# Kernel optimization log

Measured on AMD Instinct MI355X. Metric: run time of the kernel, lower is better.

The kernel has to match this reference:

```python
import jax, jax.numpy as jnp
import numpy as np

L = 3        # number of GatedGCN layers
N = 30000    # nodes
E = 480000   # edges (avg degree 16)
D = 128      # hidden dim (= in_dim = out_dim)
IN = 128     # input feature dim
G = 64       # graphs in batch
C = 10       # classes


def setup_inputs() -> dict:
    key = jax.random.key(0)
    ks = jax.random.split(key, 32)
    s = 0.05  # weight scale to keep activations / sigmoid gates in a sane range
    inp = {
        "h": jax.random.normal(ks[0], (N, IN), jnp.float32),
        "e": jax.random.normal(ks[1], (E, IN), jnp.float32),
        "snorm_n": jax.random.uniform(ks[2], (N, 1), jnp.float32),
        "snorm_e": jax.random.uniform(ks[3], (E, 1), jnp.float32),
        "src": jax.random.randint(ks[4], (E,), 0, N, jnp.int32),
        "dst": jax.random.randint(ks[5], (E,), 0, N, jnp.int32),
        "graph_id": jnp.sort(jax.random.randint(ks[6], (N,), 0, G, jnp.int32)),
        # input embeddings
        "Wh_emb": jax.random.normal(ks[7], (IN, D), jnp.float32) * s,
        "bh_emb": jnp.zeros((D,), jnp.float32),
        "We_emb": jax.random.normal(ks[8], (IN, D), jnp.float32) * s,
        "be_emb": jnp.zeros((D,), jnp.float32),
        # per-layer A,B,C,D,E linears (stacked over L)
        "WA": jax.random.normal(ks[9], (L, D, D), jnp.float32) * s,
        "bA": jnp.zeros((L, D), jnp.float32),
        "WB": jax.random.normal(ks[10], (L, D, D), jnp.float32) * s,
        "bB": jnp.zeros((L, D), jnp.float32),
        "WC": jax.random.normal(ks[11], (L, D, D), jnp.float32) * s,
        "bC": jnp.zeros((L, D), jnp.float32),
        "WD": jax.random.normal(ks[12], (L, D, D), jnp.float32) * s,
        "bD": jnp.zeros((L, D), jnp.float32),
        "WE": jax.random.normal(ks[13], (L, D, D), jnp.float32) * s,
        "bE": jnp.zeros((L, D), jnp.float32),
        # batch-norm affine params (node / edge)
        "gn_h": jnp.ones((L, D), jnp.float32),
        "bt_h": jnp.zeros((L, D), jnp.float32),
        "gn_e": jnp.ones((L, D), jnp.float32),
        "bt_e": jnp.zeros((L, D), jnp.float32),
        # readout linear
        "Wr": jax.random.normal(ks[14], (D, C), jnp.float32) * s,
        "br": jnp.zeros((C,), jnp.float32),
    }
    return inp


def _bn(x, gamma, beta):
    # training-mode BatchNorm1d: biased batch stats over the node/edge axis
    mu = jnp.mean(x, axis=0)
    var = jnp.var(x, axis=0)
    return (x - mu) * jax.lax.rsqrt(var + 1e-5) * gamma + beta


def reference(h, e, snorm_n, snorm_e, src, dst, graph_id,
              Wh_emb, bh_emb, We_emb, be_emb,
              WA, bA, WB, bB, WC, bC, WD, bD, WE, bE,
              gn_h, bt_h, gn_e, bt_e, Wr, br):
    n_nodes = h.shape[0]
    h = h @ Wh_emb + bh_emb
    e = e @ We_emb + be_emb
    for l in range(WA.shape[0]):
        h_in, e_in = h, e
        Ah = h @ WA[l] + bA[l]
        Bh = h @ WB[l] + bB[l]
        Dh = h @ WD[l] + bD[l]
        Eh = h @ WE[l] + bE[l]
        Ce = e @ WC[l] + bC[l]
        # message: e_ij = Ce + Dh_src + Eh_dst ; gate = sigmoid(e_ij)
        e_new = Ce + Dh[src] + Eh[dst]                       # [E, D]
        sig = jax.nn.sigmoid(e_new)
        # reduce at dst: gated weighted mean of Bh_src
        num = jax.ops.segment_sum(sig * Bh[src], dst, num_segments=n_nodes)
        den = jax.ops.segment_sum(sig, dst, num_segments=n_nodes)
        h_new = Ah + num / (den + 1e-6)
        # graph norm
        h_new = h_new * snorm_n
        e_new = e_new * snorm_e
        # batch norm + ReLU + residual (dropout p=0 -> identity)
        h_new = jax.nn.relu(_bn(h_new, gn_h[l], bt_h[l]))
        e_new = jax.nn.relu(_bn(e_new, gn_e[l], bt_e[l]))
        h = h_in + h_new
        e = e_in + e_new
    # mean_nodes readout per graph, then linear classifier
    sums = jax.ops.segment_sum(h, graph_id, num_segments=G)
    cnt = jax.ops.segment_sum(jnp.ones((n_nodes, 1), h.dtype), graph_id, num_segments=G)
    hg = sums / jnp.maximum(cnt, 1.0)
    return hg @ Wr + br
```

## Files before the change

### kernel.cpp

```cpp
#include <hip/hip_runtime.h>
#include <cstdint>
#include <cstddef>

#define N_NODES  30000
#define N_EDGES  480000
#define N_LAYERS 3
#define N_GRAPHS 64
#define N_CLASS  10
#define NREP     32

typedef __attribute__((ext_vector_type(8))) short short8v;
typedef __attribute__((ext_vector_type(4))) float f32x4;

__device__ __forceinline__ unsigned short f2bf(float x) {
  union { float f; unsigned u; } v; v.f = x;
  unsigned r = v.u + 0x7FFFu + ((v.u >> 16) & 1u);
  return (unsigned short)(r >> 16);
}
__device__ __forceinline__ float bf2f(unsigned short h) {
  union { unsigned u; float f; } v; v.u = ((unsigned)h) << 16;
  return v.f;
}
__device__ __forceinline__ int swzW(int row, int off16) {
  return (row << 8) | (off16 ^ ((row & 7) << 4));
}

__global__ void wconv(const float* __restrict__ Wh, const float* __restrict__ We,
                      const float* __restrict__ WA, const float* __restrict__ WB,
                      const float* __restrict__ WC, const float* __restrict__ WD,
                      const float* __restrict__ WE, unsigned short* __restrict__ Wt)
{
  const int mi  = blockIdx.x >> 6;
  const int idx = (blockIdx.x & 63) * 256 + threadIdx.x;
  const float* src;
  if      (mi == 0) src = Wh;
  else if (mi == 1) src = We;
  else if (mi < 5)  src = WA + (size_t)(mi - 2) * 16384;
  else if (mi < 8)  src = WB + (size_t)(mi - 5) * 16384;
  else if (mi < 11) src = WC + (size_t)(mi - 8) * 16384;
  else if (mi < 14) src = WD + (size_t)(mi - 11) * 16384;
  else              src = WE + (size_t)(mi - 14) * 16384;
  const int k = idx >> 7, n = idx & 127;
  Wt[(size_t)mi * 16384 + (size_t)n * 128 + k] = f2bf(src[idx]);
}

struct GemmArgs {
  const unsigned short* Wt[4];
  const float* bias[4];
  unsigned short* out[4];
};

template<int NMAT, bool AFP32>
__global__ __launch_bounds__(256)
void gemm_mm(const void* __restrict__ Ap, GemmArgs g, int M)
{
  __shared__ __align__(16) unsigned char WL[32768];
  unsigned short* Wl = (unsigned short*)WL;
  const int t = threadIdx.x;
  const int w = t >> 6, l = t & 63;
  const int lr = l & 15, lkb = (l >> 4) * 8;
  const int r0 = blockIdx.x * 64;
  int arow = r0 + w * 16 + lr; if (arow >= M) arow = M - 1;

  short8v a[4];
  if (AFP32) {
    const float* A = (const float*)Ap;
#pragma unroll
    for (int kk = 0; kk < 4; ++kk) {
      const float* p = A + (size_t)arow * 128 + kk * 32 + lkb;
      const float4 u = *(const float4*)p;
      const float4 v = *(const float4*)(p + 4);
      short8v av;
      av[0]=f2bf(u.x); av[1]=f2bf(u.y); av[2]=f2bf(u.z); av[3]=f2bf(u.w);
      av[4]=f2bf(v.x); av[5]=f2bf(v.y); av[6]=f2bf(v.z); av[7]=f2bf(v.w);
      a[kk] = av;
    }
  } else {
    const unsigned short* A = (const unsigned short*)Ap;
#pragma unroll
    for (int kk = 0; kk < 4; ++kk)
      a[kk] = *(const short8v*)(A + (size_t)arow * 128 + kk * 32 + lkb);
  }

#pragma unroll
  for (int m = 0; m < NMAT; ++m) {
    if (m) __syncthreads();
#pragma unroll
    for (int p = 0; p < 8; ++p) {
      const int ci = t + p * 256;
      *(short8v*)(WL + swzW(ci >> 4, (ci & 15) * 16)) = *(const short8v*)(g.Wt[m] + (size_t)ci * 8);
    }
    __syncthreads();
    f32x4 acc[8];
#pragma unroll
    for (int ct = 0; ct < 8; ++ct) acc[ct] = (f32x4){0.f, 0.f, 0.f, 0.f};
#pragma unroll
    for (int kk = 0; kk < 4; ++kk)
#pragma unroll
      for (int ct = 0; ct < 8; ++ct) {
        const short8v b = *(const short8v*)(WL + swzW(ct * 16 + lr, kk * 64 + (l >> 4) * 16));
        acc[ct] = __builtin_amdgcn_mfma_f32_16x16x32_bf16(a[kk], b, acc[ct], 0, 0, 0);
      }
    __syncthreads();
#pragma unroll
    for (int ct = 0; ct < 8; ++ct) {
      const float bb = g.bias[m][ct * 16 + lr];
#pragma unroll
      for (int q = 0; q < 4; ++q)
        Wl[(w * 16 + (l >> 4) * 4 + q) * 136 + ct * 16 + lr] = f2bf(acc[ct][q] + bb);
    }
    __syncthreads();
    unsigned short* out = g.out[m];
#pragma unroll
    for (int p = 0; p < 4; ++p) {
      const int ci = t + p * 256;
      const int rr = ci >> 4, co = (ci & 15) * 8;
      const int grow = r0 + rr;
      if (grow < M)
        *(short8v*)(out + (size_t)grow * 128 + co) = *(const short8v*)(Wl + rr * 136 + co);
    }
  }
}

template<int LMODE>
__global__ __launch_bounds__(256)
void edge_fused(unsigned short* __restrict__ eres, unsigned short* __restrict__ enew,
                const unsigned short* __restrict__ WtC, const float* __restrict__ bC,
                const unsigned short* __restrict__ Dh, const unsigned short* __restrict__ Eh,
                const int* __restrict__ src, const int* __restrict__ dst,
                const float* __restrict__ snorm_e, const float2* __restrict__ pq)
{
  __shared__ __align__(16) unsigned char WL[32768];
  __shared__ float2 pql[128];
  unsigned short* Wl = (unsigned short*)WL;
  const int t = threadIdx.x;
  const int w = t >> 6, l = t & 63;
  const int lr = l & 15, lkb = (l >> 4) * 8;
  const int r0 = blockIdx.x * 64;
  if (LMODE >= 1 && t < 128) pql[t] = pq[t];
#pragma unroll
  for (int p = 0; p < 8; ++p) {
    const int ci = t + p * 256;
    *(short8v*)(WL + swzW(ci >> 4, (ci & 15) * 16)) = *(const short8v*)(WtC + (size_t)ci * 8);
  }
  __syncthreads();

  const int arow = r0 + w * 16 + lr;
  short8v a[4];
  if (LMODE == 0) {
#pragma unroll
    for (int kk = 0; kk < 4; ++kk)
      a[kk] = *(const short8v*)(eres + (size_t)arow * 128 + kk * 32 + lkb);
  } else {
    const float sn = snorm_e[arow];
#pragma unroll
    for (int kk = 0; kk < 4; ++kk) {
      const short8v ep = *(const short8v*)(enew + (size_t)arow * 128 + kk * 32 + lkb);
      const short8v er = *(const short8v*)(eres + (size_t)arow * 128 + kk * 32 + lkb);
      short8v av;
#pragma unroll
      for (int j = 0; j < 8; ++j) {
        const float2 PQ = pql[kk * 32 + lkb + j];
        const float x = bf2f((unsigned short)ep[j]) * sn * PQ.x + PQ.y;
        av[j] = (short)f2bf(bf2f((unsigned short)er[j]) + fmaxf(x, 0.f));
      }
      a[kk] = av;
      if (LMODE == 1)
        *(short8v*)(eres + (size_t)arow * 128 + kk * 32 + lkb) = av;
    }
  }

  f32x4 acc[8];
#pragma unroll
  for (int ct = 0; ct < 8; ++ct) acc[ct] = (f32x4){0.f, 0.f, 0.f, 0.f};
#pragma unroll
  for (int kk = 0; kk < 4; ++kk)
#pragma unroll
    for (int ct = 0; ct < 8; ++ct) {
      const short8v b = *(const short8v*)(WL + swzW(ct * 16 + lr, kk * 64 + (l >> 4) * 16));
      acc[ct] = __builtin_amdgcn_mfma_f32_16x16x32_bf16(a[kk], b, acc[ct], 0, 0, 0);
    }
  __syncthreads();
#pragma unroll
  for (int ct = 0; ct < 8; ++ct) {
    const float bb = bC[ct * 16 + lr];
#pragma unroll
    for (int q = 0; q < 4; ++q)
      Wl[(w * 16 + (l >> 4) * 4 + q) * 136 + ct * 16 + lr] = f2bf(acc[ct][q] + bb);
  }
  __syncthreads();
#pragma unroll
  for (int p = 0; p < 4; ++p) {
    const int ci = t + p * 256;
    const int rr = ci >> 4, co = (ci & 15) * 8;
    const int edge = r0 + rr;
    const int s = src[edge], d = dst[edge];
    const short8v ce = *(const short8v*)(Wl + rr * 136 + co);
    const short8v dv = *(const short8v*)(Dh + (size_t)s * 128 + co);
    const short8v ev = *(const short8v*)(Eh + (size_t)d * 128 + co);
    short8v ov;
#pragma unroll
    for (int j = 0; j < 8; ++j)
      ov[j] = (short)f2bf(bf2f((unsigned short)ce[j]) + bf2f((unsigned short)dv[j]) + bf2f((unsigned short)ev[j]));
    *(short8v*)(enew + (size_t)edge * 128 + co) = ov;
  }
}

__global__ void hist_kernel(const int* __restrict__ dst, int* __restrict__ cnt, int E)
{
  const int i = blockIdx.x * 256 + threadIdx.x;
  if (i < E) atomicAdd(&cnt[dst[i]], 1);
}

__global__ void scan_kernel(const int* __restrict__ cnt, int* __restrict__ start,
                            int* __restrict__ cursor, int n, int total)
{
  __shared__ int lds[1024];
  const int tid = threadIdx.x;
  const int chunk = (n + 1023) / 1024;
  const int lo = tid * chunk, hi = min(lo + chunk, n);
  int s = 0;
  for (int i = lo; i < hi; ++i) s += cnt[i];
  lds[tid] = s;
  __syncthreads();
  for (int off = 1; off < 1024; off <<= 1) {
    const int v = (tid >= off) ? lds[tid - off] : 0;
    __syncthreads();
    lds[tid] += v;
    __syncthreads();
  }
  int run = (tid == 0) ? 0 : lds[tid - 1];
  for (int i = lo; i < hi; ++i) { start[i] = run; cursor[i] = run; run += cnt[i]; }
  if (tid == 0) start[n] = total;
}

__global__ void scatter_kernel(const int* __restrict__ dst, int* __restrict__ cursor,
                               int* __restrict__ csr, int E)
{
  const int i = blockIdx.x * 256 + threadIdx.x;
  if (i < E) { const int p = atomicAdd(&cursor[dst[i]], 1); csr[p] = i; }
}

__global__ __launch_bounds__(256)
void aggregate(const unsigned short* __restrict__ enew, const unsigned short* __restrict__ Bh,
               const unsigned short* __restrict__ Ah, const float* __restrict__ snorm_n,
               const float* __restrict__ snorm_e, const int* __restrict__ start,
               const int* __restrict__ csr, const int* __restrict__ src,
               float* __restrict__ tbuf, float* __restrict__ statrep, int doE)
{
  __shared__ float2 red[16][132];
  const int t = threadIdx.x;
  const int g = t >> 4, q = t & 15;
  const int v = blockIdx.x * 16 + g;
  const int s0 = start[v], s1 = start[v + 1];
  float num[8] = {0,0,0,0,0,0,0,0}, den[8] = {0,0,0,0,0,0,0,0};
  float psE[8] = {0,0,0,0,0,0,0,0}, pqE[8] = {0,0,0,0,0,0,0,0};

  float sn = 0.f;
  short8v ev = {}, bv = {};
  if (s0 < s1) {
    const int eid = csr[s0];
    const int sv  = src[eid];
    sn = snorm_e[eid];
    ev = *(const short8v*)(enew + (size_t)eid * 128 + q * 8);
    bv = *(const short8v*)(Bh + (size_t)sv * 128 + q * 8);
  }
  for (int i = s0; i < s1; ++i) {
    float snn = 0.f;
    short8v evn = {}, bvn = {};
    if (i + 1 < s1) {
      const int eid = csr[i + 1];
      const int sv  = src[eid];
      snn = snorm_e[eid];
      evn = *(const short8v*)(enew + (size_t)eid * 128 + q * 8);
      bvn = *(const short8v*)(Bh + (size_t)sv * 128 + q * 8);
    }
#pragma unroll
    for (int j = 0; j < 8; ++j) {
      const float en = bf2f((unsigned short)ev[j]);
      const float sg = 1.f / (1.f + __expf(-en));
      num[j] = fmaf(sg, bf2f((unsigned short)bv[j]), num[j]);
      den[j] += sg;
      if (doE) { const float tv = en * sn; psE[j] += tv; pqE[j] = fmaf(tv, tv, pqE[j]); }
    }
    ev = evn; bv = bvn; sn = snn;
  }
  const float snv = snorm_n[v];
  const short8v av = *(const short8v*)(Ah + (size_t)v * 128 + q * 8);
  float hv[8];
#pragma unroll
  for (int j = 0; j < 8; ++j)
    hv[j] = (bf2f((unsigned short)av[j]) + num[j] / (den[j] + 1e-6f)) * snv;
  *(float4*)(tbuf + (size_t)v * 128 + q * 8)     = make_float4(hv[0], hv[1], hv[2], hv[3]);
  *(float4*)(tbuf + (size_t)v * 128 + q * 8 + 4) = make_float4(hv[4], hv[5], hv[6], hv[7]);

  float* rep = statrep + (size_t)(blockIdx.x & (NREP - 1)) * 512;
#pragma unroll
  for (int j = 0; j < 8; ++j) red[g][q * 8 + j] = make_float2(hv[j], hv[j] * hv[j]);
  __syncthreads();
  if (t < 128) {
    float s = 0.f, qq = 0.f;
    for (int gg = 0; gg < 16; ++gg) { s += red[gg][t].x; qq += red[gg][t].y; }
    atomicAdd(rep + t, s); atomicAdd(rep + 128 + t, qq);
  }
  if (doE) {
    __syncthreads();
#pragma unroll
    for (int j = 0; j < 8; ++j) red[g][q * 8 + j] = make_float2(psE[j], pqE[j]);
    __syncthreads();
    if (t < 128) {
      float s = 0.f, qq = 0.f;
      for (int gg = 0; gg < 16; ++gg) { s += red[gg][t].x; qq += red[gg][t].y; }
      atomicAdd(rep + 256 + t, s); atomicAdd(rep + 384 + t, qq);
    }
  }
}

__global__ void finalize_kernel(const float* __restrict__ rep, float* __restrict__ mu,
                                float2* __restrict__ pq, const float* __restrict__ gn_e_l,
                                const float* __restrict__ bt_e_l, float invN, float invE)
{
  const int c = threadIdx.x;
  float sH = 0.f, qH = 0.f, sE = 0.f, qE = 0.f;
  for (int r = 0; r < NREP; ++r) {
    const float* p = rep + (size_t)r * 512;
    sH += p[c]; qH += p[128 + c]; sE += p[256 + c]; qE += p[384 + c];
  }
  const float muH = sH * invN;
  const float vH  = fmaxf(qH * invN - muH * muH, 0.f);
  mu[c]       = muH;
  mu[128 + c] = rsqrtf(vH + 1e-5f);
  const float muE = sE * invE;
  const float vE  = fmaxf(qE * invE - muE * muE, 0.f);
  const float P   = rsqrtf(vE + 1e-5f) * gn_e_l[c];
  pq[c] = make_float2(P, bt_e_l[c] - muE * P);
}

__global__ __launch_bounds__(256)
void node_apply(unsigned short* __restrict__ h, const float* __restrict__ tb,
                const float* __restrict__ mu, const float* __restrict__ gn,
                const float* __restrict__ bt)
{
  const int i = blockIdx.x * 256 + threadIdx.x;
  const int c0 = (i & 15) * 8;
  const float* tp = tb + (size_t)i * 8;
  short8v hv = *(short8v*)(h + (size_t)i * 8);
#pragma unroll
  for (int j = 0; j < 8; ++j) {
    const int c = c0 + j;
    const float x = (tp[j] - mu[c]) * mu[128 + c] * gn[c] + bt[c];
    hv[j] = (short)f2bf(bf2f((unsigned short)hv[j]) + fmaxf(x, 0.f));
  }
  *(short8v*)(h + (size_t)i * 8) = hv;
}

__global__ void readout_scatter(const unsigned short* __restrict__ h, const int* __restrict__ gid,
                                float* __restrict__ gsum, int* __restrict__ gcnt, int N)
{
  const int c = threadIdx.x;
  const int row0 = blockIdx.x * 256;
  int cur = -1, cnt = 0;
  float s = 0.f;
  for (int r = 0; r < 256; ++r) {
    const int v = row0 + r;
    if (v >= N) break;
    const int g = gid[v];
    if (g != cur) {
      if (cur >= 0) {
        atomicAdd(&gsum[(size_t)cur * 128 + c], s);
        if (c == 0) atomicAdd(&gcnt[cur], cnt);
      }
      cur = g; s = 0.f; cnt = 0;
    }
    s += bf2f(h[(size_t)v * 128 + c]);
    ++cnt;
  }
  if (cur >= 0) {
    atomicAdd(&gsum[(size_t)cur * 128 + c], s);
    if (c == 0) atomicAdd(&gcnt[cur], cnt);
  }
}

__global__ void readout_final(const float* __restrict__ gsum, const int* __restrict__ gcnt,
                              const float* __restrict__ Wr, const float* __restrict__ br,
                              float* __restrict__ out)
{
  const int g = blockIdx.x;
  const int t = threadIdx.x;
  __shared__ float hg[128];
  const float cnt = fmaxf((float)gcnt[g], 1.f);
  hg[t] = gsum[(size_t)g * 128 + t] / cnt;
  __syncthreads();
  if (t < N_CLASS) {
    float acc = br[t];
    for (int k = 0; k < 128; ++k) acc = fmaf(hg[k], Wr[k * N_CLASS + t], acc);
    out[g * N_CLASS + t] = acc;
  }
}

extern "C" void kernel_launch(void* const* d_in, const int* in_sizes, int n_in,
                              void* d_out, int out_size, void* d_ws, size_t ws_size,
                              hipStream_t stream)
{
  const float* h_in    = (const float*)d_in[0];
  const float* e_in    = (const float*)d_in[1];
  const float* snorm_n = (const float*)d_in[2];
  const float* snorm_e = (const float*)d_in[3];
  const int*   src     = (const int*)d_in[4];
  const int*   dst     = (const int*)d_in[5];
  const int*   gid     = (const int*)d_in[6];
  const float* Wh_emb  = (const float*)d_in[7];
  const float* bh_emb  = (const float*)d_in[8];
  const float* We_emb  = (const float*)d_in[9];
  const float* be_emb  = (const float*)d_in[10];
  const float* WA = (const float*)d_in[11]; const float* bA = (const float*)d_in[12];
  const float* WB = (const float*)d_in[13]; const float* bB = (const float*)d_in[14];
  const float* WC = (const float*)d_in[15]; const float* bC = (const float*)d_in[16];
  const float* WD = (const float*)d_in[17]; const float* bD = (const float*)d_in[18];
  const float* WE = (const float*)d_in[19]; const float* bE = (const float*)d_in[20];
  const float* gn_h = (const float*)d_in[21]; const float* bt_h = (const float*)d_in[22];
  const float* gn_e = (const float*)d_in[23]; const float* bt_e = (const float*)d_in[24];
  const float* Wr = (const float*)d_in[25]; const float* br = (const float*)d_in[26];
  float* out = (float*)d_out;
  (void)in_sizes; (void)n_in; (void)out_size; (void)ws_size;

  char* ws = (char*)d_ws;
  size_t off = 0;
  auto alloc = [&](size_t bytes) -> char* {
    off = (off + 255) & ~(size_t)255;
    char* p = ws + off;
    off += bytes;
    return p;
  };
  const size_t ND = (size_t)N_NODES * 128, ED = (size_t)N_EDGES * 128;
  unsigned short* hbuf = (unsigned short*)alloc(ND * 2);
  unsigned short* ebuf = (unsigned short*)alloc(ED * 2);
  unsigned short* enew = (unsigned short*)alloc(ED * 2);
  unsigned short* Ah   = (unsigned short*)alloc(ND * 2);
  unsigned short* Bh   = (unsigned short*)alloc(ND * 2);
  unsigned short* Dh   = (unsigned short*)alloc(ND * 2);
  unsigned short* Eh   = (unsigned short*)alloc(ND * 2);
  float* tbuf          = (float*)alloc(ND * 4);
  unsigned short* Wt   = (unsigned short*)alloc((size_t)17 * 16384 * 2);
  float* statrep       = (float*)alloc((size_t)NREP * 512 * 4);
  float* mu            = (float*)alloc(256 * 4);
  float2* pq           = (float2*)alloc(128 * 8);
  int* cnt    = (int*)alloc((size_t)N_NODES * 4);
  int* start  = (int*)alloc((size_t)(N_NODES + 1) * 4);
  int* cursor = (int*)alloc((size_t)N_NODES * 4);
  int* csr    = (int*)alloc((size_t)N_EDGES * 4);
  float* gsum = (float*)alloc((size_t)N_GRAPHS * 128 * 4);
  int* gcnt   = (int*)alloc((size_t)N_GRAPHS * 4);

  wconv<<<17 * 64, 256, 0, stream>>>(Wh_emb, We_emb, WA, WB, WC, WD, WE, Wt);

  hipMemsetAsync(cnt, 0, (size_t)N_NODES * 4, stream);
  hist_kernel<<<(N_EDGES + 255) / 256, 256, 0, stream>>>(dst, cnt, N_EDGES);
  scan_kernel<<<1, 1024, 0, stream>>>(cnt, start, cursor, N_NODES, N_EDGES);
  scatter_kernel<<<(N_EDGES + 255) / 256, 256, 0, stream>>>(dst, cursor, csr, N_EDGES);

  const int gbN = (N_NODES + 63) / 64;
  const int gbE = N_EDGES / 64;

  {
    GemmArgs g{};
    g.Wt[0] = Wt + 0 * 16384; g.bias[0] = bh_emb; g.out[0] = hbuf;
    gemm_mm<1, true><<<gbN, 256, 0, stream>>>(h_in, g, N_NODES);
    g.Wt[0] = Wt + 1 * 16384; g.bias[0] = be_emb; g.out[0] = ebuf;
    gemm_mm<1, true><<<gbE, 256, 0, stream>>>(e_in, g, N_EDGES);
  }

  for (int l = 0; l < N_LAYERS; ++l) {
    const size_t bOff = (size_t)l * 128;
    const int doE = (l < N_LAYERS - 1) ? 1 : 0;
    {
      GemmArgs g{};
      g.Wt[0] = Wt + (size_t)(2 + l)  * 16384; g.bias[0] = bA + bOff; g.out[0] = Ah;
      g.Wt[1] = Wt + (size_t)(5 + l)  * 16384; g.bias[1] = bB + bOff; g.out[1] = Bh;
      g.Wt[2] = Wt + (size_t)(11 + l) * 16384; g.bias[2] = bD + bOff; g.out[2] = Dh;
      g.Wt[3] = Wt + (size_t)(14 + l) * 16384; g.bias[3] = bE + bOff; g.out[3] = Eh;
      gemm_mm<4, false><<<gbN, 256, 0, stream>>>(hbuf, g, N_NODES);
    }
    const unsigned short* WtC = Wt + (size_t)(8 + l) * 16384;
    if (l == 0)
      edge_fused<0><<<gbE, 256, 0, stream>>>(ebuf, enew, WtC, bC + bOff, Dh, Eh, src, dst, snorm_e, pq);
    else if (l == 1)
      edge_fused<1><<<gbE, 256, 0, stream>>>(ebuf, enew, WtC, bC + bOff, Dh, Eh, src, dst, snorm_e, pq);
    else
      edge_fused<2><<<gbE, 256, 0, stream>>>(ebuf, enew, WtC, bC + bOff, Dh, Eh, src, dst, snorm_e, pq);
    hipMemsetAsync(statrep, 0, (size_t)NREP * 512 * 4, stream);
    aggregate<<<N_NODES / 16, 256, 0, stream>>>(enew, Bh, Ah, snorm_n, snorm_e,
                                                start, csr, src, tbuf, statrep, doE);
    finalize_kernel<<<1, 128, 0, stream>>>(statrep, mu, pq, gn_e + bOff, bt_e + bOff,
                                           1.f / N_NODES, 1.f / N_EDGES);
    node_apply<<<N_NODES / 16, 256, 0, stream>>>(hbuf, tbuf, mu, gn_h + bOff, bt_h + bOff);
  }

  hipMemsetAsync(gsum, 0, (size_t)N_GRAPHS * 128 * 4, stream);
  hipMemsetAsync(gcnt, 0, (size_t)N_GRAPHS * 4, stream);
  readout_scatter<<<(N_NODES + 255) / 256, 128, 0, stream>>>(hbuf, gid, gsum, gcnt, N_NODES);
  readout_final<<<N_GRAPHS, 128, 0, stream>>>(gsum, gcnt, Wr, br, out);
}
```

Before: 902.0 us.

## Fuse node BN apply into GEMMs, widen edge tiles, pre-permute CSR edge data

```diff
diff --git a/kernel.cpp b/kernel.cpp
--- a/kernel.cpp
+++ b/kernel.cpp
@@ -50,9 +50,11 @@
   unsigned short* out[4];
 };
 
-template<int NMAT, bool AFP32>
+template<int NMAT, bool AFP32, bool APPLY>
 __global__ __launch_bounds__(256)
-void gemm_mm(const void* __restrict__ Ap, GemmArgs g, int M)
+void gemm_mm(const void* __restrict__ Ap, GemmArgs g, int M,
+             const float* __restrict__ tb, const float2* __restrict__ pqh,
+             unsigned short* __restrict__ hout)
 {
   __shared__ __align__(16) unsigned char WL[32768];
   unsigned short* Wl = (unsigned short*)WL;
@@ -60,6 +62,7 @@
   const int w = t >> 6, l = t & 63;
   const int lr = l & 15, lkb = (l >> 4) * 8;
   const int r0 = blockIdx.x * 64;
+  const bool vrow = (r0 + w * 16 + lr) < M;
   int arow = r0 + w * 16 + lr; if (arow >= M) arow = M - 1;
 
   short8v a[4];
@@ -75,6 +78,25 @@
       av[4]=f2bf(v.x); av[5]=f2bf(v.y); av[6]=f2bf(v.z); av[7]=f2bf(v.w);
       a[kk] = av;
     }
+  } else if (APPLY) {
+    const unsigned short* A = (const unsigned short*)Ap;
+#pragma unroll
+    for (int kk = 0; kk < 4; ++kk) {
+      const float* tp = tb + (size_t)arow * 128 + kk * 32 + lkb;
+      const float4 t0 = *(const float4*)tp;
+      const float4 t1 = *(const float4*)(tp + 4);
+      const short8v hr = *(const short8v*)(A + (size_t)arow * 128 + kk * 32 + lkb);
+      const float tt[8] = {t0.x,t0.y,t0.z,t0.w,t1.x,t1.y,t1.z,t1.w};
+      short8v av;
+#pragma unroll
+      for (int j = 0; j < 8; ++j) {
+        const float2 PQ = pqh[kk * 32 + lkb + j];
+        const float x = tt[j] * PQ.x + PQ.y;
+        av[j] = (short)f2bf(bf2f((unsigned short)hr[j]) + fmaxf(x, 0.f));
+      }
+      a[kk] = av;
+      if (vrow) *(short8v*)(hout + (size_t)arow * 128 + kk * 32 + lkb) = av;
+    }
   } else {
     const unsigned short* A = (const unsigned short*)Ap;
 #pragma unroll
@@ -124,85 +146,122 @@
 
 template<int LMODE>
 __global__ __launch_bounds__(256)
-void edge_fused(unsigned short* __restrict__ eres, unsigned short* __restrict__ enew,
-                const unsigned short* __restrict__ WtC, const float* __restrict__ bC,
-                const unsigned short* __restrict__ Dh, const unsigned short* __restrict__ Eh,
-                const int* __restrict__ src, const int* __restrict__ dst,
-                const float* __restrict__ snorm_e, const float2* __restrict__ pq)
-{
-  __shared__ __align__(16) unsigned char WL[32768];
+void edge_kern(const void* __restrict__ Ap, unsigned short* __restrict__ eres,
+               unsigned short* __restrict__ enew,
+               const unsigned short* __restrict__ Wt, const float* __restrict__ bias,
+               const unsigned short* __restrict__ Dh, const unsigned short* __restrict__ Eh,
+               const int* __restrict__ src, const int* __restrict__ dst,
+               const float* __restrict__ snorm_e, const float2* __restrict__ pq)
+{
+  __shared__ __align__(16) unsigned char SM[33792];
   __shared__ float2 pql[128];
-  unsigned short* Wl = (unsigned short*)WL;
+  unsigned short* TB = (unsigned short*)SM;
   const int t = threadIdx.x;
   const int w = t >> 6, l = t & 63;
   const int lr = l & 15, lkb = (l >> 4) * 8;
-  const int r0 = blockIdx.x * 64;
-  if (LMODE >= 1 && t < 128) pql[t] = pq[t];
+  const int r0 = blockIdx.x * 128;
+  if (LMODE >= 2 && t < 128) pql[t] = pq[t];
 #pragma unroll
   for (int p = 0; p < 8; ++p) {
     const int ci = t + p * 256;
-    *(short8v*)(WL + swzW(ci >> 4, (ci & 15) * 16)) = *(const short8v*)(WtC + (size_t)ci * 8);
+    *(short8v*)(SM + swzW(ci >> 4, (ci & 15) * 16)) = *(const short8v*)(Wt + (size_t)ci * 8);
+  }
+
+  short8v a[2][4];
+  if (LMODE == 0) {
+    const float* A = (const float*)Ap;
+#pragma unroll
+    for (int mt = 0; mt < 2; ++mt) {
+      const int arow = r0 + w * 32 + mt * 16 + lr;
+#pragma unroll
+      for (int kk = 0; kk < 4; ++kk) {
+        const float* p2 = A + (size_t)arow * 128 + kk * 32 + lkb;
+        const float4 u = *(const float4*)p2;
+        const float4 v = *(const float4*)(p2 + 4);
+        short8v av;
+        av[0]=f2bf(u.x); av[1]=f2bf(u.y); av[2]=f2bf(u.z); av[3]=f2bf(u.w);
+        av[4]=f2bf(v.x); av[5]=f2bf(v.y); av[6]=f2bf(v.z); av[7]=f2bf(v.w);
+        a[mt][kk] = av;
+      }
+    }
+  } else if (LMODE == 1) {
+    const unsigned short* A = (const unsigned short*)Ap;
+#pragma unroll
+    for (int mt = 0; mt < 2; ++mt) {
+      const int arow = r0 + w * 32 + mt * 16 + lr;
+#pragma unroll
+      for (int kk = 0; kk < 4; ++kk)
+        a[mt][kk] = *(const short8v*)(A + (size_t)arow * 128 + kk * 32 + lkb);
+    }
   }
   __syncthreads();
 
-  const int arow = r0 + w * 16 + lr;
-  short8v a[4];
-  if (LMODE == 0) {
-#pragma unroll
-    for (int kk = 0; kk < 4; ++kk)
-      a[kk] = *(const short8v*)(eres + (size_t)arow * 128 + kk * 32 + lkb);
-  } else {
-    const float sn = snorm_e[arow];
-#pragma unroll
-    for (int kk = 0; kk < 4; ++kk) {
-      const short8v ep = *(const short8v*)(enew + (size_t)arow * 128 + kk * 32 + lkb);
-      const short8v er = *(const short8v*)(eres + (size_t)arow * 128 + kk * 32 + lkb);
-      short8v av;
-#pragma unroll
-      for (int j = 0; j < 8; ++j) {
-        const float2 PQ = pql[kk * 32 + lkb + j];
-        const float x = bf2f((unsigned short)ep[j]) * sn * PQ.x + PQ.y;
-        av[j] = (short)f2bf(bf2f((unsigned short)er[j]) + fmaxf(x, 0.f));
+  if (LMODE >= 2) {
+    const unsigned short* A = (const unsigned short*)Ap;
+#pragma unroll
+    for (int mt = 0; mt < 2; ++mt) {
+      const int arow = r0 + w * 32 + mt * 16 + lr;
+      const float sn = snorm_e[arow];
+#pragma unroll
+      for (int kk = 0; kk < 4; ++kk) {
+        const short8v ep = *(const short8v*)(enew + (size_t)arow * 128 + kk * 32 + lkb);
+        const short8v er = *(const short8v*)(A + (size_t)arow * 128 + kk * 32 + lkb);
+        short8v av;
+#pragma unroll
+        for (int j = 0; j < 8; ++j) {
+          const float2 PQ = pql[kk * 32 + lkb + j];
+          const float x = bf2f((unsigned short)ep[j]) * sn * PQ.x + PQ.y;
+          av[j] = (short)f2bf(bf2f((unsigned short)er[j]) + fmaxf(x, 0.f));
+        }
+        a[mt][kk] = av;
+        if (LMODE == 2)
+          *(short8v*)(eres + (size_t)arow * 128 + kk * 32 + lkb) = av;
       }
-      a[kk] = av;
-      if (LMODE == 1)
-        *(short8v*)(eres + (size_t)arow * 128 + kk * 32 + lkb) = av;
-    }
-  }
-
-  f32x4 acc[8];
-#pragma unroll
-  for (int ct = 0; ct < 8; ++ct) acc[ct] = (f32x4){0.f, 0.f, 0.f, 0.f};
+    }
+  }
+
+  f32x4 acc[2][8];
+#pragma unroll
+  for (int mt = 0; mt < 2; ++mt)
+#pragma unroll
+    for (int ct = 0; ct < 8; ++ct) acc[mt][ct] = (f32x4){0.f, 0.f, 0.f, 0.f};
 #pragma unroll
   for (int kk = 0; kk < 4; ++kk)
 #pragma unroll
     for (int ct = 0; ct < 8; ++ct) {
-      const short8v b = *(const short8v*)(WL + swzW(ct * 16 + lr, kk * 64 + (l >> 4) * 16));
-      acc[ct] = __builtin_amdgcn_mfma_f32_16x16x32_bf16(a[kk], b, acc[ct], 0, 0, 0);
+      const short8v b = *(const short8v*)(SM + swzW(ct * 16 + lr, kk * 64 + (l >> 4) * 16));
+      acc[0][ct] = __builtin_amdgcn_mfma_f32_16x16x32_bf16(a[0][kk], b, acc[0][ct], 0, 0, 0);
+      acc[1][ct] = __builtin_amdgcn_mfma_f32_16x16x32_bf16(a[1][kk], b, acc[1][ct], 0, 0, 0);
     }
   __syncthreads();
 #pragma unroll
   for (int ct = 0; ct < 8; ++ct) {
-    const float bb = bC[ct * 16 + lr];
-#pragma unroll
-    for (int q = 0; q < 4; ++q)
-      Wl[(w * 16 + (l >> 4) * 4 + q) * 136 + ct * 16 + lr] = f2bf(acc[ct][q] + bb);
+    const float bb = bias[ct * 16 + lr];
+#pragma unroll
+    for (int mt = 0; mt < 2; ++mt)
+#pragma unroll
+      for (int q = 0; q < 4; ++q)
+        TB[(w * 32 + mt * 16 + (l >> 4) * 4 + q) * 132 + ct * 16 + lr] = f2bf(acc[mt][ct][q] + bb);
   }
   __syncthreads();
 #pragma unroll
-  for (int p = 0; p < 4; ++p) {
+  for (int p = 0; p < 8; ++p) {
     const int ci = t + p * 256;
     const int rr = ci >> 4, co = (ci & 15) * 8;
     const int edge = r0 + rr;
-    const int s = src[edge], d = dst[edge];
-    const short8v ce = *(const short8v*)(Wl + rr * 136 + co);
-    const short8v dv = *(const short8v*)(Dh + (size_t)s * 128 + co);
-    const short8v ev = *(const short8v*)(Eh + (size_t)d * 128 + co);
-    short8v ov;
-#pragma unroll
-    for (int j = 0; j < 8; ++j)
-      ov[j] = (short)f2bf(bf2f((unsigned short)ce[j]) + bf2f((unsigned short)dv[j]) + bf2f((unsigned short)ev[j]));
-    *(short8v*)(enew + (size_t)edge * 128 + co) = ov;
+    const short8v ce = *(const short8v*)(TB + rr * 132 + co);
+    if (LMODE == 0) {
+      *(short8v*)(eres + (size_t)edge * 128 + co) = ce;
+    } else {
+      const int s = src[edge], d = dst[edge];
+      const short8v dv = *(const short8v*)(Dh + (size_t)s * 128 + co);
+      const short8v ev = *(const short8v*)(Eh + (size_t)d * 128 + co);
+      short8v ov;
+#pragma unroll
+      for (int j = 0; j < 8; ++j)
+        ov[j] = (short)f2bf(bf2f((unsigned short)ce[j]) + bf2f((unsigned short)dv[j]) + bf2f((unsigned short)ev[j]));
+      *(short8v*)(enew + (size_t)edge * 128 + co) = ov;
+    }
   }
 }
 
@@ -234,18 +293,23 @@
   if (tid == 0) start[n] = total;
 }
 
-__global__ void scatter_kernel(const int* __restrict__ dst, int* __restrict__ cursor,
-                               int* __restrict__ csr, int E)
+__global__ void scatter_kernel(const int* __restrict__ dst, const int* __restrict__ src,
+                               const float* __restrict__ sne, int* __restrict__ cursor,
+                               int* __restrict__ csr, int* __restrict__ csrc,
+                               float* __restrict__ csne, int E)
 {
   const int i = blockIdx.x * 256 + threadIdx.x;
-  if (i < E) { const int p = atomicAdd(&cursor[dst[i]], 1); csr[p] = i; }
+  if (i < E) {
+    const int p = atomicAdd(&cursor[dst[i]], 1);
+    csr[p] = i; csrc[p] = src[i]; csne[p] = sne[i];
+  }
 }
 
 __global__ __launch_bounds__(256)
 void aggregate(const unsigned short* __restrict__ enew, const unsigned short* __restrict__ Bh,
                const unsigned short* __restrict__ Ah, const float* __restrict__ snorm_n,
-               const float* __restrict__ snorm_e, const int* __restrict__ start,
-               const int* __restrict__ csr, const int* __restrict__ src,
+               const int* __restrict__ start, const int* __restrict__ csr,
+               const int* __restrict__ csrc, const float* __restrict__ csne,
                float* __restrict__ tbuf, float* __restrict__ statrep, int doE)
 {
   __shared__ float2 red[16][132];
@@ -260,20 +324,18 @@
   short8v ev = {}, bv = {};
   if (s0 < s1) {
     const int eid = csr[s0];
-    const int sv  = src[eid];
-    sn = snorm_e[eid];
+    sn = csne[s0];
     ev = *(const short8v*)(enew + (size_t)eid * 128 + q * 8);
-    bv = *(const short8v*)(Bh + (size_t)sv * 128 + q * 8);
+    bv = *(const short8v*)(Bh + (size_t)csrc[s0] * 128 + q * 8);
   }
   for (int i = s0; i < s1; ++i) {
     float snn = 0.f;
     short8v evn = {}, bvn = {};
     if (i + 1 < s1) {
       const int eid = csr[i + 1];
-      const int sv  = src[eid];
-      snn = snorm_e[eid];
+      snn = csne[i + 1];
       evn = *(const short8v*)(enew + (size_t)eid * 128 + q * 8);
-      bvn = *(const short8v*)(Bh + (size_t)sv * 128 + q * 8);
+      bvn = *(const short8v*)(Bh + (size_t)csrc[i + 1] * 128 + q * 8);
     }
 #pragma unroll
     for (int j = 0; j < 8; ++j) {
@@ -316,48 +378,37 @@
   }
 }
 
-__global__ void finalize_kernel(const float* __restrict__ rep, float* __restrict__ mu,
-                                float2* __restrict__ pq, const float* __restrict__ gn_e_l,
-                                const float* __restrict__ bt_e_l, float invN, float invE)
+__global__ void finalize_kernel(float* __restrict__ rep, float2* __restrict__ pqh,
+                                float2* __restrict__ pqe,
+                                const float* __restrict__ gn_h_l, const float* __restrict__ bt_h_l,
+                                const float* __restrict__ gn_e_l, const float* __restrict__ bt_e_l,
+                                float invN, float invE, int doE)
 {
   const int c = threadIdx.x;
   float sH = 0.f, qH = 0.f, sE = 0.f, qE = 0.f;
   for (int r = 0; r < NREP; ++r) {
-    const float* p = rep + (size_t)r * 512;
+    float* p = rep + (size_t)r * 512;
     sH += p[c]; qH += p[128 + c]; sE += p[256 + c]; qE += p[384 + c];
+    p[c] = 0.f; p[128 + c] = 0.f; p[256 + c] = 0.f; p[384 + c] = 0.f;
   }
   const float muH = sH * invN;
   const float vH  = fmaxf(qH * invN - muH * muH, 0.f);
-  mu[c]       = muH;
-  mu[128 + c] = rsqrtf(vH + 1e-5f);
-  const float muE = sE * invE;
-  const float vE  = fmaxf(qE * invE - muE * muE, 0.f);
-  const float P   = rsqrtf(vE + 1e-5f) * gn_e_l[c];
-  pq[c] = make_float2(P, bt_e_l[c] - muE * P);
-}
-
-__global__ __launch_bounds__(256)
-void node_apply(unsigned short* __restrict__ h, const float* __restrict__ tb,
-                const float* __restrict__ mu, const float* __restrict__ gn,
-                const float* __restrict__ bt)
-{
-  const int i = blockIdx.x * 256 + threadIdx.x;
-  const int c0 = (i & 15) * 8;
-  const float* tp = tb + (size_t)i * 8;
-  short8v hv = *(short8v*)(h + (size_t)i * 8);
-#pragma unroll
-  for (int j = 0; j < 8; ++j) {
-    const int c = c0 + j;
-    const float x = (tp[j] - mu[c]) * mu[128 + c] * gn[c] + bt[c];
-    hv[j] = (short)f2bf(bf2f((unsigned short)hv[j]) + fmaxf(x, 0.f));
-  }
-  *(short8v*)(h + (size_t)i * 8) = hv;
-}
-
-__global__ void readout_scatter(const unsigned short* __restrict__ h, const int* __restrict__ gid,
+  const float PH  = rsqrtf(vH + 1e-5f) * gn_h_l[c];
+  pqh[c] = make_float2(PH, bt_h_l[c] - muH * PH);
+  if (doE) {
+    const float muE = sE * invE;
+    const float vE  = fmaxf(qE * invE - muE * muE, 0.f);
+    const float PE  = rsqrtf(vE + 1e-5f) * gn_e_l[c];
+    pqe[c] = make_float2(PE, bt_e_l[c] - muE * PE);
+  }
+}
+
+__global__ void readout_scatter(const unsigned short* __restrict__ h, const float* __restrict__ tb,
+                                const float2* __restrict__ pqh, const int* __restrict__ gid,
                                 float* __restrict__ gsum, int* __restrict__ gcnt, int N)
 {
   const int c = threadIdx.x;
+  const float2 PQ = pqh[c];
   const int row0 = blockIdx.x * 256;
   int cur = -1, cnt = 0;
   float s = 0.f;
@@ -372,7 +423,7 @@
       }
       cur = g; s = 0.f; cnt = 0;
     }
-    s += bf2f(h[(size_t)v * 128 + c]);
+    s += bf2f(h[(size_t)v * 128 + c]) + fmaxf(tb[(size_t)v * 128 + c] * PQ.x + PQ.y, 0.f);
     ++cnt;
   }
   if (cur >= 0) {
@@ -443,32 +494,36 @@
   float* tbuf          = (float*)alloc(ND * 4);
   unsigned short* Wt   = (unsigned short*)alloc((size_t)17 * 16384 * 2);
   float* statrep       = (float*)alloc((size_t)NREP * 512 * 4);
-  float* mu            = (float*)alloc(256 * 4);
-  float2* pq           = (float2*)alloc(128 * 8);
+  float2* pqh          = (float2*)alloc(128 * 8);
+  float2* pqe          = (float2*)alloc(128 * 8);
   int* cnt    = (int*)alloc((size_t)N_NODES * 4);
   int* start  = (int*)alloc((size_t)(N_NODES + 1) * 4);
   int* cursor = (int*)alloc((size_t)N_NODES * 4);
   int* csr    = (int*)alloc((size_t)N_EDGES * 4);
+  int* csrc   = (int*)alloc((size_t)N_EDGES * 4);
+  float* csne = (float*)alloc((size_t)N_EDGES * 4);
   float* gsum = (float*)alloc((size_t)N_GRAPHS * 128 * 4);
   int* gcnt   = (int*)alloc((size_t)N_GRAPHS * 4);
 
   wconv<<<17 * 64, 256, 0, stream>>>(Wh_emb, We_emb, WA, WB, WC, WD, WE, Wt);
 
   hipMemsetAsync(cnt, 0, (size_t)N_NODES * 4, stream);
+  hipMemsetAsync(statrep, 0, (size_t)NREP * 512 * 4, stream);
   hist_kernel<<<(N_EDGES + 255) / 256, 256, 0, stream>>>(dst, cnt, N_EDGES);
   scan_kernel<<<1, 1024, 0, stream>>>(cnt, start, cursor, N_NODES, N_EDGES);
-  scatter_kernel<<<(N_EDGES + 255) / 256, 256, 0, stream>>>(dst, cursor, csr, N_EDGES);
+  scatter_kernel<<<(N_EDGES + 255) / 256, 256, 0, stream>>>(dst, src, snorm_e, cursor,
+                                                            csr, csrc, csne, N_EDGES);
 
   const int gbN = (N_NODES + 63) / 64;
-  const int gbE = N_EDGES / 64;
+  const int gbE = N_EDGES / 128;
 
   {
     GemmArgs g{};
     g.Wt[0] = Wt + 0 * 16384; g.bias[0] = bh_emb; g.out[0] = hbuf;
-    gemm_mm<1, true><<<gbN, 256, 0, stream>>>(h_in, g, N_NODES);
-    g.Wt[0] = Wt + 1 * 16384; g.bias[0] = be_emb; g.out[0] = ebuf;
-    gemm_mm<1, true><<<gbE, 256, 0, stream>>>(e_in, g, N_EDGES);
-  }
+    gemm_mm<1, true, false><<<gbN, 256, 0, stream>>>(h_in, g, N_NODES, nullptr, nullptr, nullptr);
+  }
+  edge_kern<0><<<gbE, 256, 0, stream>>>(e_in, ebuf, nullptr, Wt + 1 * 16384, be_emb,
+                                        nullptr, nullptr, nullptr, nullptr, nullptr, nullptr);
 
   for (int l = 0; l < N_LAYERS; ++l) {
     const size_t bOff = (size_t)l * 128;
@@ -479,25 +534,29 @@
       g.Wt[1] = Wt + (size_t)(5 + l)  * 16384; g.bias[1] = bB + bOff; g.out[1] = Bh;
       g.Wt[2] = Wt + (size_t)(11 + l) * 16384; g.bias[2] = bD + bOff; g.out[2] = Dh;
       g.Wt[3] = Wt + (size_t)(14 + l) * 16384; g.bias[3] = bE + bOff; g.out[3] = Eh;
-      gemm_mm<4, false><<<gbN, 256, 0, stream>>>(hbuf, g, N_NODES);
+      if (l == 0)
+        gemm_mm<4, false, false><<<gbN, 256, 0, stream>>>(hbuf, g, N_NODES, nullptr, nullptr, nullptr);
+      else
+        gemm_mm<4, false, true><<<gbN, 256, 0, stream>>>(hbuf, g, N_NODES, tbuf, pqh, hbuf);
     }
     const unsigned short* WtC = Wt + (size_t)(8 + l) * 16384;
     if (l == 0)
-      edge_fused<0><<<gbE, 256, 0, stream>>>(ebuf, enew, WtC, bC + bOff, Dh, Eh, src, dst, snorm_e, pq);
+      edge_kern<1><<<gbE, 256, 0, stream>>>(ebuf, nullptr, enew, WtC, bC + bOff,
+                                            Dh, Eh, src, dst, nullptr, nullptr);
     else if (l == 1)
-      edge_fused<1><<<gbE, 256, 0, stream>>>(ebuf, enew, WtC, bC + bOff, Dh, Eh, src, dst, snorm_e, pq);
+      edge_kern<2><<<gbE, 256, 0, stream>>>(ebuf, ebuf, enew, WtC, bC + bOff,
+                                            Dh, Eh, src, dst, snorm_e, pqe);
     else
-      edge_fused<2><<<gbE, 256, 0, stream>>>(ebuf, enew, WtC, bC + bOff, Dh, Eh, src, dst, snorm_e, pq);
-    hipMemsetAsync(statrep, 0, (size_t)NREP * 512 * 4, stream);
-    aggregate<<<N_NODES / 16, 256, 0, stream>>>(enew, Bh, Ah, snorm_n, snorm_e,
-                                                start, csr, src, tbuf, statrep, doE);
-    finalize_kernel<<<1, 128, 0, stream>>>(statrep, mu, pq, gn_e + bOff, bt_e + bOff,
-                                           1.f / N_NODES, 1.f / N_EDGES);
-    node_apply<<<N_NODES / 16, 256, 0, stream>>>(hbuf, tbuf, mu, gn_h + bOff, bt_h + bOff);
-  }
-
-  hipMemsetAsync(gsum, 0, (size_t)N_GRAPHS * 128 * 4, stream);
-  hipMemsetAsync(gcnt, 0, (size_t)N_GRAPHS * 4, stream);
-  readout_scatter<<<(N_NODES + 255) / 256, 128, 0, stream>>>(hbuf, gid, gsum, gcnt, N_NODES);
+      edge_kern<3><<<gbE, 256, 0, stream>>>(ebuf, nullptr, enew, WtC, bC + bOff,
+                                            Dh, Eh, src, dst, snorm_e, pqe);
+    aggregate<<<N_NODES / 16, 256, 0, stream>>>(enew, Bh, Ah, snorm_n,
+                                                start, csr, csrc, csne, tbuf, statrep, doE);
+    finalize_kernel<<<1, 128, 0, stream>>>(statrep, pqh, pqe, gn_h + bOff, bt_h + bOff,
+                                           gn_e + bOff, bt_e + bOff,
+                                           1.f / N_NODES, 1.f / N_EDGES, doE);
+  }
+
+  hipMemsetAsync(gsum, 0, (size_t)N_GRAPHS * 128 * 4 + (size_t)N_GRAPHS * 4, stream);
+  readout_scatter<<<(N_NODES + 255) / 256, 128, 0, stream>>>(hbuf, tbuf, pqh, gid, gsum, gcnt, N_NODES);
   readout_final<<<N_GRAPHS, 128, 0, stream>>>(gsum, gcnt, Wr, br, out);
 }
```

After: 984.9 us. +9.2%, slower.
